# Kernel tuning notes

Hardware: AMD Instinct MI355X
Metric: run time of the kernel (lower is better)

The kernel has to match this reference:

```python
import jax, jax.numpy as jnp
import numpy as np

B, S, D, H = 8, 1024, 768, 12
DH = D // H  # 64
PATCHES = S  # module's `patches` arg; rows >= patches//2 are zeroed pre-softmax


def setup_inputs() -> dict:
    key = jax.random.key(0)
    ks = jax.random.split(key, 5)
    sc = 1.0 / np.sqrt(D)
    return {
        "hidden_states": jax.random.normal(ks[0], (B, S, D), dtype=jnp.float32),
        "Wq": jax.random.normal(ks[1], (D, D), dtype=jnp.float32) * sc,
        "bq": jnp.zeros((D,), dtype=jnp.float32),
        "Wk": jax.random.normal(ks[2], (D, D), dtype=jnp.float32) * sc,
        "bk": jnp.zeros((D,), dtype=jnp.float32),
        "Wv": jax.random.normal(ks[3], (D, D), dtype=jnp.float32) * sc,
        "bv": jnp.zeros((D,), dtype=jnp.float32),
        "Wo": jax.random.normal(ks[4], (D, D), dtype=jnp.float32) * sc,
        "bo": jnp.zeros((D,), dtype=jnp.float32),
    }


def _split_heads(x):
    # [B,S,D] -> [B,H,S,DH]
    b, s, _ = x.shape
    return x.reshape(b, s, H, DH).transpose(0, 2, 1, 3)


def reference(hidden_states, Wq, bq, Wk, bk, Wv, bv, Wo, bo):
    # self-attention path (kv=None), mask=None path, eval-mode dropout (identity)
    q = _split_heads(hidden_states @ Wq + bq)
    k = _split_heads(hidden_states @ Wk + bk)
    v = _split_heads(hidden_states @ Wv + bv)
    scores = jnp.einsum("bhqd,bhkd->bhqk", q, k) / np.sqrt(DH)
    # custom masking: zero out all score rows for query positions >= patches//2
    scores = scores.at[:, :, PATCHES // 2 :, :].set(0.0)
    probs = jax.nn.softmax(scores, axis=-1)
    ctx = jnp.einsum("bhqk,bhkd->bhqd", probs, v)
    ctx = ctx.transpose(0, 2, 1, 3).reshape(hidden_states.shape[0], -1, D)
    return ctx @ Wo + bo  # vis=False -> weights not returned
```

## Files before the change

kernel.cpp:

```cpp
#include <hip/hip_runtime.h>
#include <hip/hip_bf16.h>
#include <cstdint>


typedef __bf16 bf16_t;
typedef bf16_t bf16x8 __attribute__((ext_vector_type(8)));
typedef float f32x4 __attribute__((ext_vector_type(4)));

#define QSCALE 0.18033688011112042f

__device__ __forceinline__ f32x4 mfma16(bf16x8 a, bf16x8 b, f32x4 c) {
  return __builtin_amdgcn_mfma_f32_16x16x32_bf16(a, b, c, 0, 0, 0);
}
__device__ __forceinline__ unsigned packbf(float x, float y) {
  union { bf16_t h; unsigned short u; } a, b;
  a.h = (bf16_t)x; b.h = (bf16_t)y;
  return (unsigned)a.u | ((unsigned)b.u << 16);
}
__device__ __forceinline__ unsigned short tobf(float x) {
  union { bf16_t h; unsigned short u; } a; a.h = (bf16_t)x; return a.u;
}
__device__ __forceinline__ void glds16(const void* g, void* s) {
  __builtin_amdgcn_global_load_lds((const __attribute__((address_space(1))) void*)g,
                                   (__attribute__((address_space(3))) void*)s, 16, 0, 0);
}

__global__ __launch_bounds__(256) void k_prep(const float* __restrict__ X,
                                              const float* __restrict__ Wq,
                                              const float* __restrict__ Wk,
                                              const float* __restrict__ Wv,
                                              const float* __restrict__ Wo,
                                              unsigned short* __restrict__ Xbf,
                                              unsigned short* __restrict__ Wt) {
  __shared__ float tile[64][65];
  if (blockIdx.x < 3072) {
    int i = blockIdx.x * 256 + threadIdx.x;
    const float4* p = (const float4*)X;
    float4 a = p[2 * i], b = p[2 * i + 1];
    uint4 o;
    o.x = packbf(a.x, a.y); o.y = packbf(a.z, a.w);
    o.z = packbf(b.x, b.y); o.w = packbf(b.z, b.w);
    ((uint4*)Xbf)[i] = o;
    return;
  }
  int id = blockIdx.x - 3072;
  int which = id / 144;
  int rem = id - which * 144;
  const float* W = (which == 0) ? Wq : (which == 1) ? Wk : (which == 2) ? Wv : Wo;
  int k0 = (rem / 12) * 64, n0 = (rem % 12) * 64;
  int t = threadIdx.x;
  int c = t & 63, r0 = t >> 6;
#pragma unroll
  for (int i = 0; i < 16; ++i) {
    int r = r0 + i * 4;
    tile[r][c] = W[(size_t)(k0 + r) * 768 + n0 + c];
  }
  __syncthreads();
#pragma unroll
  for (int i = 0; i < 16; ++i) {
    int nr = r0 + i * 4;
    Wt[(size_t)(which * 768 + n0 + nr) * 768 + k0 + c] = tobf(tile[c][nr]);
  }
}

__global__ __launch_bounds__(256) void k_gemm_qkv(
    const unsigned short* __restrict__ Xbf, const unsigned short* __restrict__ Wt,
    const float* __restrict__ bq, const float* __restrict__ bk, const float* __restrict__ bv,
    unsigned short* __restrict__ Qw, unsigned short* __restrict__ Kw,
    unsigned short* __restrict__ Vt) {
  __shared__ __align__(16) unsigned short As[8192], Bs[8192];
  int id = blockIdx.x;
  int mt, nt;
  if (id < 576) { int mf = id / 18; mt = ((mf >> 2) << 3) + (mf & 3); nt = id - mf * 18; }
  else { int j = id - 576; int mh = j / 12; mt = ((mh >> 2) << 3) + 4 + (mh & 3); nt = 6 + (j - mh * 12); }
  const int m0 = mt * 128, n0 = nt * 128;
  const int tid = threadIdx.x, w = tid >> 6, l = tid & 63, lr = l & 15, lg = l >> 4;
  const int wm = w >> 1, wn = w & 1;
  const unsigned short* gA = Xbf + (size_t)(m0 + (l >> 2)) * 768 + (l & 3) * 8;
  const unsigned short* gB = Wt + (size_t)(n0 + (l >> 2)) * 768 + (l & 3) * 8;
  const size_t rlo = (size_t)(w * 16) * 768, rhi = (size_t)((4 + w) * 16) * 768;
  unsigned short* sA0 = As + w * 512;
  unsigned short* sB0 = Bs + w * 512;
  const unsigned short* rA = As + (wm * 64 + lr) * 32 + lg * 8;
  const unsigned short* rB = Bs + (wn * 64 + lr) * 32 + lg * 8;
  f32x4 acc[4][4] = {};
  for (int kt = 0; kt < 12; ++kt) {
    const int ko = kt * 64;
    glds16(gA + rlo + ko, sA0);            glds16(gA + rhi + ko, sA0 + 2048);
    glds16(gA + rlo + ko + 32, sA0 + 4096); glds16(gA + rhi + ko + 32, sA0 + 6144);
    glds16(gB + rlo + ko, sB0);            glds16(gB + rhi + ko, sB0 + 2048);
    glds16(gB + rlo + ko + 32, sB0 + 4096); glds16(gB + rhi + ko + 32, sB0 + 6144);
    __syncthreads();
#pragma unroll
    for (int kh = 0; kh < 2; ++kh) {
      bf16x8 af[4], bfr[4];
#pragma unroll
      for (int i = 0; i < 4; ++i) af[i] = *(const bf16x8*)(rA + kh * 4096 + i * 512);
#pragma unroll
      for (int i = 0; i < 4; ++i) bfr[i] = *(const bf16x8*)(rB + kh * 4096 + i * 512);
#pragma unroll
      for (int i = 0; i < 4; ++i)
#pragma unroll
        for (int j = 0; j < 4; ++j) acc[i][j] = mfma16(af[i], bfr[j], acc[i][j]);
    }
    __syncthreads();
  }
  const int rbase = m0 + wm * 64 + lg * 4;
  const int cbase = n0 + wn * 64 + lr;
#pragma unroll
  for (int nf = 0; nf < 4; ++nf) {
    const int n = cbase + nf * 16;
#pragma unroll
    for (int mf = 0; mf < 4; ++mf) {
      const int r = rbase + mf * 16;
      const int b = r >> 10, s = r & 1023;
      if (n < 768) {
        const int h = n >> 6, dh = n & 63;
        const float bias = bq[n];
        unsigned short* qp = Qw + ((size_t)(b * 12 + h) * 512 + s) * 64 + dh;
#pragma unroll
        for (int rg = 0; rg < 4; ++rg)
          qp[(size_t)rg * 64] = tobf((acc[mf][nf][rg] + bias) * QSCALE);
      } else if (n < 1536) {
        const int d = n - 768, h = d >> 6, dh = d & 63;
        const float bias = bk[d];
        unsigned short* kp = Kw + ((size_t)(b * 12 + h) * 1024 + s) * 64 + dh;
#pragma unroll
        for (int rg = 0; rg < 4; ++rg)
          kp[(size_t)rg * 64] = tobf(acc[mf][nf][rg] + bias);
      } else {
        const int d = n - 1536, h = d >> 6, dh = d & 63;
        const float bias = bv[d];
        uint2 pv;
        pv.x = packbf(acc[mf][nf][0] + bias, acc[mf][nf][1] + bias);
        pv.y = packbf(acc[mf][nf][2] + bias, acc[mf][nf][3] + bias);
        *(uint2*)(Vt + ((size_t)(b * 12 + h) * 64 + dh) * 1024 + s) = pv;
      }
    }
  }
}

__global__ __launch_bounds__(256) void k_attn(const unsigned short* __restrict__ Qw,
                                              const unsigned short* __restrict__ Kw,
                                              const unsigned short* __restrict__ Vt,
                                              unsigned short* __restrict__ Ctx,
                                              float* __restrict__ mv) {
  const int id = blockIdx.x;
  const int bh = id % 96;
  const int q0 = (id / 96) * 64;
  const int tid = threadIdx.x, w = tid >> 6, l = tid & 63, lr = l & 15, lg = l >> 4;
  const unsigned short* Qp = Qw + (size_t)bh * 512 * 64;
  const unsigned short* Kp = Kw + (size_t)bh * 1024 * 64;
  const unsigned short* Vp = Vt + (size_t)bh * 64 * 1024;

  __shared__ __align__(16) unsigned short Ks[2][4096];
  __shared__ __align__(16) unsigned short Vs[2][4096];
  __shared__ __align__(16) unsigned short P[4 * 16 * 72];

  const int j1 = 2 * w, j2 = 2 * w + 1;
  const int rA = j1 * 8 + (l >> 3), cA = (l & 7) ^ (rA & 7);
  const int rB = j2 * 8 + (l >> 3), cB = (l & 7) ^ (rB & 7);
  const unsigned short* kSrcA = Kp + rA * 64 + cA * 8;
  const unsigned short* kSrcB = Kp + rB * 64 + cB * 8;
  const unsigned short* vSrcA = Vp + rA * 1024 + cA * 8;
  const unsigned short* vSrcB = Vp + rB * 1024 + cB * 8;

  const int s0 = lr * 64 + ((lg ^ (lr & 7)) * 8);
  const int s1 = lr * 64 + (((lg + 4) ^ (lr & 7)) * 8);

  unsigned short* prow = P + (w * 16 + lr) * 72;
  const unsigned short* prd = prow + lg * 8;
  const int qrow = q0 + w * 16 + lr;
  const bf16x8 qf0 = *(const bf16x8*)(Qp + (size_t)qrow * 64 + lg * 8);
  const bf16x8 qf1 = *(const bf16x8*)(Qp + (size_t)qrow * 64 + 32 + lg * 8);

  f32x4 accc[4] = {};
  float vs0 = 0.f, vs1 = 0.f, vs2 = 0.f, vs3 = 0.f;
  float z = 0.f;

  glds16(kSrcA, &Ks[0][j1 * 512]);
  glds16(kSrcB, &Ks[0][j2 * 512]);
  glds16(vSrcA, &Vs[0][j1 * 512]);
  glds16(vSrcB, &Vs[0][j2 * 512]);
  __syncthreads();

  for (int t = 0; t < 16; ++t) {
    const int pcur = t & 1;
    if (t < 15) {
      const int kv0 = (t + 1) * 64;
      glds16(kSrcA + (size_t)kv0 * 64, &Ks[1 - pcur][j1 * 512]);
      glds16(kSrcB + (size_t)kv0 * 64, &Ks[1 - pcur][j2 * 512]);
      glds16(vSrcA + kv0, &Vs[1 - pcur][j1 * 512]);
      glds16(vSrcB + kv0, &Vs[1 - pcur][j2 * 512]);
    }
    const unsigned short* Kb = Ks[pcur];
    const unsigned short* Vb = Vs[pcur];
    f32x4 ss[4] = {};
#pragma unroll
    for (int m = 0; m < 4; ++m) {
      bf16x8 k0 = *(const bf16x8*)(Kb + m * 1024 + s0);
      bf16x8 k1 = *(const bf16x8*)(Kb + m * 1024 + s1);
      ss[m] = mfma16(k0, qf0, ss[m]);
      ss[m] = mfma16(k1, qf1, ss[m]);
    }
#pragma unroll
    for (int m = 0; m < 4; ++m) {
      float p0 = exp2f(ss[m][0]), p1 = exp2f(ss[m][1]);
      float p2 = exp2f(ss[m][2]), p3 = exp2f(ss[m][3]);
      z += (p0 + p1) + (p2 + p3);
      uint2 pw;
      pw.x = packbf(p0, p1); pw.y = packbf(p2, p3);
      *(uint2*)(prow + m * 16 + lg * 4) = pw;
    }
    bf16x8 pb0 = *(const bf16x8*)prd;
    bf16x8 pb1 = *(const bf16x8*)(prd + 32);
#pragma unroll
    for (int m = 0; m < 4; ++m) {
      bf16x8 v0 = *(const bf16x8*)(Vb + m * 1024 + s0);
      bf16x8 v1 = *(const bf16x8*)(Vb + m * 1024 + s1);
      if (id < 96) {
        float sv = 0.f;
#pragma unroll
        for (int jj = 0; jj < 8; ++jj) sv += (float)v0[jj] + (float)v1[jj];
        if (m == 0) vs0 += sv; else if (m == 1) vs1 += sv;
        else if (m == 2) vs2 += sv; else vs3 += sv;
      }
      accc[m] = mfma16(v0, pb0, accc[m]);
      accc[m] = mfma16(v1, pb1, accc[m]);
    }
    __syncthreads();
  }

  const int b = bh / 12, h = bh - b * 12;
  if (id < 96) {
    vs0 += __shfl_xor(vs0, 16, 64); vs0 += __shfl_xor(vs0, 32, 64);
    vs1 += __shfl_xor(vs1, 16, 64); vs1 += __shfl_xor(vs1, 32, 64);
    vs2 += __shfl_xor(vs2, 16, 64); vs2 += __shfl_xor(vs2, 32, 64);
    vs3 += __shfl_xor(vs3, 16, 64); vs3 += __shfl_xor(vs3, 32, 64);
    if (w == 0 && lg == 0) {
      float* mp = mv + b * 768 + h * 64 + lr;
      mp[0] = vs0 * (1.f / 1024.f);
      mp[16] = vs1 * (1.f / 1024.f);
      mp[32] = vs2 * (1.f / 1024.f);
      mp[48] = vs3 * (1.f / 1024.f);
    }
  }

  z += __shfl_xor(z, 16, 64);
  z += __shfl_xor(z, 32, 64);
  const float zinv = 1.0f / z;
  unsigned short* crow = Ctx + ((size_t)b * 512 + qrow) * 768 + h * 64 + lg * 4;
#pragma unroll
  for (int m = 0; m < 4; ++m) {
    uint2 pv;
    pv.x = packbf(accc[m][0] * zinv, accc[m][1] * zinv);
    pv.y = packbf(accc[m][2] * zinv, accc[m][3] * zinv);
    *(uint2*)(crow + m * 16) = pv;
  }
}

__global__ __launch_bounds__(256) void k_tail(const float* __restrict__ mv,
                                              const float* __restrict__ Wo,
                                              const float* __restrict__ bo,
                                              float* __restrict__ out) {
  const int b = blockIdx.x, n0 = blockIdx.y * 128;
  const int tid = threadIdx.x;
  __shared__ float mvs[768];
  __shared__ float cvals[128];
  for (int i = tid; i < 768; i += 256) mvs[i] = mv[b * 768 + i];
  __syncthreads();
  const int col = n0 + (tid >> 1);
  const int half = tid & 1;
  float a = 0.f;
  const int kend = half * 384 + 384;
  for (int k = half * 384; k < kend; ++k)
    a += mvs[k] * Wo[(size_t)k * 768 + col];
  a += __shfl_xor(a, 1, 64);
  if (half == 0) cvals[col - n0] = a + bo[col];
  __syncthreads();
  const float4 c4 = ((const float4*)cvals)[tid & 31];
  const int srow = tid >> 5;
  float* obase = out + ((size_t)b * 1024 + 512 + srow) * 768 + n0;
  for (int r = 0; r < 512; r += 8)
    ((float4*)(obase + (size_t)r * 768))[tid & 31] = c4;
}

__global__ __launch_bounds__(256) void k_gemm_o(const unsigned short* __restrict__ Ctx,
                                                const unsigned short* __restrict__ WtO,
                                                const float* __restrict__ bo,
                                                float* __restrict__ out) {
  __shared__ __align__(16) unsigned short As[4096], Bs[4096];
  const int m0 = blockIdx.x * 128, n0 = blockIdx.y * 128;
  const int tid = threadIdx.x, w = tid >> 6, l = tid & 63, lr = l & 15, lg = l >> 4;
  const int wm = w >> 1, wn = w & 1;
  const unsigned short* gA = Ctx + (size_t)(m0 + (tid >> 2)) * 768 + (tid & 3) * 8;
  const unsigned short* gB = WtO + (size_t)(n0 + (tid >> 2)) * 768 + (tid & 3) * 8;
  unsigned short* sA = As + w * 512;
  unsigned short* sB = Bs + w * 512;
  const unsigned short* rA = As + (wm * 64 + lr) * 32 + lg * 8;
  const unsigned short* rB = Bs + (wn * 64 + lr) * 32 + lg * 8;
  f32x4 acc[4][4] = {};
  for (int kt = 0; kt < 24; ++kt) {
    const int ko = kt * 32;
    glds16(gA + ko, sA);            glds16(gA + 64 * 768 + ko, sA + 2048);
    glds16(gB + ko, sB);            glds16(gB + 64 * 768 + ko, sB + 2048);
    __syncthreads();
    bf16x8 af[4], bfr[4];
#pragma unroll
    for (int i = 0; i < 4; ++i) af[i] = *(const bf16x8*)(rA + i * 512);
#pragma unroll
    for (int i = 0; i < 4; ++i) bfr[i] = *(const bf16x8*)(rB + i * 512);
#pragma unroll
    for (int i = 0; i < 4; ++i)
#pragma unroll
      for (int j = 0; j < 4; ++j) acc[i][j] = mfma16(af[i], bfr[j], acc[i][j]);
    __syncthreads();
  }
  const int rbase = m0 + wm * 64 + lg * 4;
  const int cbase = n0 + wn * 64 + lr;
#pragma unroll
  for (int nf = 0; nf < 4; ++nf) {
    const int n = cbase + nf * 16;
    const float bias = bo[n];
#pragma unroll
    for (int mf = 0; mf < 4; ++mf) {
      const int r = rbase + mf * 16;
      const int b = r >> 9, s = r & 511;
      float* op = out + ((size_t)b * 1024 + s) * 768 + n;
#pragma unroll
      for (int rg = 0; rg < 4; ++rg) op[(size_t)rg * 768] = acc[mf][nf][rg] + bias;
    }
  }
}

extern "C" void kernel_launch(void* const* d_in, const int* in_sizes, int n_in,
                              void* d_out, int out_size, void* d_ws, size_t ws_size,
                              hipStream_t stream) {
  const float* X  = (const float*)d_in[0];
  const float* Wq = (const float*)d_in[1];
  const float* bq = (const float*)d_in[2];
  const float* Wk = (const float*)d_in[3];
  const float* bk = (const float*)d_in[4];
  const float* Wv = (const float*)d_in[5];
  const float* bv = (const float*)d_in[6];
  const float* Wo = (const float*)d_in[7];
  const float* bo = (const float*)d_in[8];
  float* out = (float*)d_out;
  char* ws = (char*)d_ws;

  unsigned short* Xbf = (unsigned short*)(ws);
  unsigned short* Wt  = (unsigned short*)(ws + 12582912);
  unsigned short* Qw  = (unsigned short*)(ws + 17301504);
  unsigned short* Kw  = (unsigned short*)(ws + 23592960);
  unsigned short* Vt  = (unsigned short*)(ws + 36175872);
  unsigned short* Ctx = (unsigned short*)(ws + 48758784);
  float* mv   = (float*)(ws + 55050240);

  k_prep<<<3648, 256, 0, stream>>>(X, Wq, Wk, Wv, Wo, Xbf, Wt);
  k_gemm_qkv<<<960, 256, 0, stream>>>(Xbf, Wt, bq, bk, bv, Qw, Kw, Vt);
  k_attn<<<768, 256, 0, stream>>>(Qw, Kw, Vt, Ctx, mv);
  k_tail<<<dim3(8, 6), 256, 0, stream>>>(mv, Wo, bo, out);
  k_gemm_o<<<dim3(32, 6), 256, 0, stream>>>(Ctx, Wt + (size_t)2304 * 768, bo, out);
}
```

Measured before the change: 213.8 us.

## Double-buffer QKV and O GEMM tiles and merge tail into O GEMM launch

Both the QKV and the output-projection GEMMs now use two shared-memory buffers. The next 32-wide K slice is loaded directly into LDS while the current one feeds MFMA, which hides global-to-LDS latency behind compute. The separate k_tail kernel, which handles the constant second half of the rows, is folded into the k_gemm_o launch as extra blocks, so one kernel launch goes away and the two pieces of work run concurrently. In exchange, the GEMM blocks use more LDS and the merged kernel is more complex, which may lower occupancy.

```diff
diff --git a/kernel.cpp b/kernel.cpp
--- a/kernel.cpp
+++ b/kernel.cpp
@@ -68,7 +68,7 @@
     const float* __restrict__ bq, const float* __restrict__ bk, const float* __restrict__ bv,
     unsigned short* __restrict__ Qw, unsigned short* __restrict__ Kw,
     unsigned short* __restrict__ Vt) {
-  __shared__ __align__(16) unsigned short As[8192], Bs[8192];
+  __shared__ __align__(16) unsigned short As0[4096], Bs0[4096], As1[4096], Bs1[4096];
   int id = blockIdx.x;
   int mt, nt;
   if (id < 576) { int mf = id / 18; mt = ((mf >> 2) << 3) + (mf & 3); nt = id - mf * 18; }
@@ -76,35 +76,46 @@
   const int m0 = mt * 128, n0 = nt * 128;
   const int tid = threadIdx.x, w = tid >> 6, l = tid & 63, lr = l & 15, lg = l >> 4;
   const int wm = w >> 1, wn = w & 1;
-  const unsigned short* gA = Xbf + (size_t)(m0 + (l >> 2)) * 768 + (l & 3) * 8;
-  const unsigned short* gB = Wt + (size_t)(n0 + (l >> 2)) * 768 + (l & 3) * 8;
-  const size_t rlo = (size_t)(w * 16) * 768, rhi = (size_t)((4 + w) * 16) * 768;
-  unsigned short* sA0 = As + w * 512;
-  unsigned short* sB0 = Bs + w * 512;
-  const unsigned short* rA = As + (wm * 64 + lr) * 32 + lg * 8;
-  const unsigned short* rB = Bs + (wn * 64 + lr) * 32 + lg * 8;
+  const unsigned short* gA = Xbf + (size_t)(m0 + (tid >> 2)) * 768 + (tid & 3) * 8;
+  const unsigned short* gB = Wt + (size_t)(n0 + (tid >> 2)) * 768 + (tid & 3) * 8;
+  const int woff = w * 512;
+  const int rAo = (wm * 64 + lr) * 32 + lg * 8;
+  const int rBo = (wn * 64 + lr) * 32 + lg * 8;
   f32x4 acc[4][4] = {};
-  for (int kt = 0; kt < 12; ++kt) {
-    const int ko = kt * 64;
-    glds16(gA + rlo + ko, sA0);            glds16(gA + rhi + ko, sA0 + 2048);
-    glds16(gA + rlo + ko + 32, sA0 + 4096); glds16(gA + rhi + ko + 32, sA0 + 6144);
-    glds16(gB + rlo + ko, sB0);            glds16(gB + rhi + ko, sB0 + 2048);
-    glds16(gB + rlo + ko + 32, sB0 + 4096); glds16(gB + rhi + ko + 32, sB0 + 6144);
-    __syncthreads();
-#pragma unroll
-    for (int kh = 0; kh < 2; ++kh) {
-      bf16x8 af[4], bfr[4];
-#pragma unroll
-      for (int i = 0; i < 4; ++i) af[i] = *(const bf16x8*)(rA + kh * 4096 + i * 512);
-#pragma unroll
-      for (int i = 0; i < 4; ++i) bfr[i] = *(const bf16x8*)(rB + kh * 4096 + i * 512);
-#pragma unroll
-      for (int i = 0; i < 4; ++i)
-#pragma unroll
-        for (int j = 0; j < 4; ++j) acc[i][j] = mfma16(af[i], bfr[j], acc[i][j]);
-    }
-    __syncthreads();
-  }
+
+#define QKV_STAGE(bufA, bufB, ko)                                              \
+  {                                                                            \
+    glds16(gA + (ko), bufA + woff);                                            \
+    glds16(gA + 64 * 768 + (ko), bufA + woff + 2048);                          \
+    glds16(gB + (ko), bufB + woff);                                            \
+    glds16(gB + 64 * 768 + (ko), bufB + woff + 2048);                          \
+  }
+#define QKV_COMPUTE(bufA, bufB)                                                \
+  {                                                                            \
+    bf16x8 af[4], bfr[4];                                                      \
+    _Pragma("unroll") for (int i = 0; i < 4; ++i)                              \
+      af[i] = *(const bf16x8*)(bufA + rAo + i * 512);                          \
+    _Pragma("unroll") for (int i = 0; i < 4; ++i)                              \
+      bfr[i] = *(const bf16x8*)(bufB + rBo + i * 512);                         \
+    _Pragma("unroll") for (int i = 0; i < 4; ++i)                              \
+      _Pragma("unroll") for (int j = 0; j < 4; ++j)                            \
+        acc[i][j] = mfma16(af[i], bfr[j], acc[i][j]);                          \
+  }
+
+  QKV_STAGE(As0, Bs0, 0);
+  __syncthreads();
+  for (int kk = 0; kk < 12; ++kk) {
+    const int ko = kk * 64;
+    QKV_STAGE(As1, Bs1, ko + 32);
+    QKV_COMPUTE(As0, Bs0);
+    __syncthreads();
+    if (kk < 11) { QKV_STAGE(As0, Bs0, ko + 64); }
+    QKV_COMPUTE(As1, Bs1);
+    __syncthreads();
+  }
+#undef QKV_STAGE
+#undef QKV_COMPUTE
+
   const int rbase = m0 + wm * 64 + lg * 4;
   const int cbase = n0 + wn * 64 + lr;
 #pragma unroll
@@ -259,63 +270,80 @@
   }
 }
 
-__global__ __launch_bounds__(256) void k_tail(const float* __restrict__ mv,
-                                              const float* __restrict__ Wo,
-                                              const float* __restrict__ bo,
-                                              float* __restrict__ out) {
-  const int b = blockIdx.x, n0 = blockIdx.y * 128;
-  const int tid = threadIdx.x;
+__global__ __launch_bounds__(256) void k_gemm_o(const unsigned short* __restrict__ Ctx,
+                                                const unsigned short* __restrict__ WtO,
+                                                const float* __restrict__ mv,
+                                                const float* __restrict__ Wo,
+                                                const float* __restrict__ bo,
+                                                float* __restrict__ out) {
+  __shared__ __align__(16) unsigned short As0[4096], Bs0[4096], As1[4096], Bs1[4096];
   __shared__ float mvs[768];
   __shared__ float cvals[128];
-  for (int i = tid; i < 768; i += 256) mvs[i] = mv[b * 768 + i];
-  __syncthreads();
-  const int col = n0 + (tid >> 1);
-  const int half = tid & 1;
-  float a = 0.f;
-  const int kend = half * 384 + 384;
-  for (int k = half * 384; k < kend; ++k)
-    a += mvs[k] * Wo[(size_t)k * 768 + col];
-  a += __shfl_xor(a, 1, 64);
-  if (half == 0) cvals[col - n0] = a + bo[col];
-  __syncthreads();
-  const float4 c4 = ((const float4*)cvals)[tid & 31];
-  const int srow = tid >> 5;
-  float* obase = out + ((size_t)b * 1024 + 512 + srow) * 768 + n0;
-  for (int r = 0; r < 512; r += 8)
-    ((float4*)(obase + (size_t)r * 768))[tid & 31] = c4;
-}
-
-__global__ __launch_bounds__(256) void k_gemm_o(const unsigned short* __restrict__ Ctx,
-                                                const unsigned short* __restrict__ WtO,
-                                                const float* __restrict__ bo,
-                                                float* __restrict__ out) {
-  __shared__ __align__(16) unsigned short As[4096], Bs[4096];
-  const int m0 = blockIdx.x * 128, n0 = blockIdx.y * 128;
-  const int tid = threadIdx.x, w = tid >> 6, l = tid & 63, lr = l & 15, lg = l >> 4;
+  const int tid = threadIdx.x;
+  if (blockIdx.x >= 192) {
+    const int tb = blockIdx.x - 192;
+    const int b = tb / 6, n0 = (tb - b * 6) * 128;
+    for (int i = tid; i < 768; i += 256) mvs[i] = mv[b * 768 + i];
+    __syncthreads();
+    const int col = n0 + (tid >> 1);
+    const int half = tid & 1;
+    float a = 0.f;
+    const int kend = half * 384 + 384;
+    for (int k = half * 384; k < kend; ++k)
+      a += mvs[k] * Wo[(size_t)k * 768 + col];
+    a += __shfl_xor(a, 1, 64);
+    if (half == 0) cvals[col - n0] = a + bo[col];
+    __syncthreads();
+    const float4 c4 = ((const float4*)cvals)[tid & 31];
+    const int srow = tid >> 5;
+    float* obase = out + ((size_t)b * 1024 + 512 + srow) * 768 + n0;
+    for (int r = 0; r < 512; r += 8)
+      ((float4*)(obase + (size_t)r * 768))[tid & 31] = c4;
+    return;
+  }
+  const int m0 = (blockIdx.x / 6) * 128, n0 = (blockIdx.x % 6) * 128;
+  const int w = tid >> 6, l = tid & 63, lr = l & 15, lg = l >> 4;
   const int wm = w >> 1, wn = w & 1;
   const unsigned short* gA = Ctx + (size_t)(m0 + (tid >> 2)) * 768 + (tid & 3) * 8;
   const unsigned short* gB = WtO + (size_t)(n0 + (tid >> 2)) * 768 + (tid & 3) * 8;
-  unsigned short* sA = As + w * 512;
-  unsigned short* sB = Bs + w * 512;
-  const unsigned short* rA = As + (wm * 64 + lr) * 32 + lg * 8;
-  const unsigned short* rB = Bs + (wn * 64 + lr) * 32 + lg * 8;
+  const int woff = w * 512;
+  const int rAo = (wm * 64 + lr) * 32 + lg * 8;
+  const int rBo = (wn * 64 + lr) * 32 + lg * 8;
   f32x4 acc[4][4] = {};
-  for (int kt = 0; kt < 24; ++kt) {
-    const int ko = kt * 32;
-    glds16(gA + ko, sA);            glds16(gA + 64 * 768 + ko, sA + 2048);
-    glds16(gB + ko, sB);            glds16(gB + 64 * 768 + ko, sB + 2048);
-    __syncthreads();
-    bf16x8 af[4], bfr[4];
-#pragma unroll
-    for (int i = 0; i < 4; ++i) af[i] = *(const bf16x8*)(rA + i * 512);
-#pragma unroll
-    for (int i = 0; i < 4; ++i) bfr[i] = *(const bf16x8*)(rB + i * 512);
-#pragma unroll
-    for (int i = 0; i < 4; ++i)
-#pragma unroll
-      for (int j = 0; j < 4; ++j) acc[i][j] = mfma16(af[i], bfr[j], acc[i][j]);
-    __syncthreads();
-  }
+
+#define O_STAGE(bufA, bufB, ko)                                                \
+  {                                                                            \
+    glds16(gA + (ko), bufA + woff);                                            \
+    glds16(gA + 64 * 768 + (ko), bufA + woff + 2048);                          \
+    glds16(gB + (ko), bufB + woff);                                            \
+    glds16(gB + 64 * 768 + (ko), bufB + woff + 2048);                          \
+  }
+#define O_COMPUTE(bufA, bufB)                                                  \
+  {                                                                            \
+    bf16x8 af[4], bfr[4];                                                      \
+    _Pragma("unroll") for (int i = 0; i < 4; ++i)                              \
+      af[i] = *(const bf16x8*)(bufA + rAo + i * 512);                          \
+    _Pragma("unroll") for (int i = 0; i < 4; ++i)                              \
+      bfr[i] = *(const bf16x8*)(bufB + rBo + i * 512);                         \
+    _Pragma("unroll") for (int i = 0; i < 4; ++i)                              \
+      _Pragma("unroll") for (int j = 0; j < 4; ++j)                            \
+        acc[i][j] = mfma16(af[i], bfr[j], acc[i][j]);                          \
+  }
+
+  O_STAGE(As0, Bs0, 0);
+  __syncthreads();
+  for (int kk = 0; kk < 12; ++kk) {
+    const int ko = kk * 64;
+    O_STAGE(As1, Bs1, ko + 32);
+    O_COMPUTE(As0, Bs0);
+    __syncthreads();
+    if (kk < 11) { O_STAGE(As0, Bs0, ko + 64); }
+    O_COMPUTE(As1, Bs1);
+    __syncthreads();
+  }
+#undef O_STAGE
+#undef O_COMPUTE
+
   const int rbase = m0 + wm * 64 + lg * 4;
   const int cbase = n0 + wn * 64 + lr;
 #pragma unroll
@@ -359,6 +387,5 @@
   k_prep<<<3648, 256, 0, stream>>>(X, Wq, Wk, Wv, Wo, Xbf, Wt);
   k_gemm_qkv<<<960, 256, 0, stream>>>(Xbf, Wt, bq, bk, bv, Qw, Kw, Vt);
   k_attn<<<768, 256, 0, stream>>>(Qw, Kw, Vt, Ctx, mv);
-  k_tail<<<dim3(8, 6), 256, 0, stream>>>(mv, Wo, bo, out);
-  k_gemm_o<<<dim3(32, 6), 256, 0, stream>>>(Ctx, Wt + (size_t)2304 * 768, bo, out);
-}
+  k_gemm_o<<<240, 256, 0, stream>>>(Ctx, Wt + (size_t)2304 * 768, mv, Wo, bo, out);
+}
```

Result: faster. 201.6 us (-5.7%).
